# Kernel optimization log

Measured on AMD Instinct MI355X. Metric: run time of the kernel, lower is better.

The kernel has to match this reference:

```python
import math
import jax, jax.numpy as jnp
import numpy as np

B, T, D_MODEL, H, D = 2, 1024, 1024, 16, 64
NUM_LEVELS = int(math.ceil(math.log2(T + 1))) + 1  # 12 for max_seq_len=1024


def _fenwick_level(idx):
    return (idx & -idx).bit_length() - 1


def build_fenwick_masks(T, num_levels):
    """NumPy replica of the torch build_fenwick_masks; returns [L, T, T] float32."""
    j_to_nodes = {}
    for j in range(1, T + 1):
        nodes = []
        idx = j
        while idx <= T:
            nodes.append((idx, _fenwick_level(idx)))
            idx += idx & -idx
        j_to_nodes[j] = nodes
    t_to_query_nodes = {}
    for t in range(1, T + 1):
        s = set()
        idx = t
        while idx > 0:
            s.add(idx)
            idx -= idx & -idx
        t_to_query_nodes[t] = s
    masks = np.zeros((num_levels, T, T), dtype=np.float32)
    for t in range(1, T + 1):
        qn = t_to_query_nodes[t]
        for j in range(1, t + 1):
            for node_idx, node_level in j_to_nodes[j]:
                if node_idx in qn:
                    masks[min(node_level, num_levels - 1), t - 1, j - 1] = 1.0
                    break
    return masks


def setup_inputs() -> dict:
    key = jax.random.key(0)
    ks = jax.random.split(key, 8)
    s = 0.02
    return {
        "x": jax.random.normal(ks[0], (B, T, D_MODEL), jnp.float32),
        "qw": jax.random.normal(ks[1], (D_MODEL, H * D), jnp.float32) * s,
        "qb": jnp.zeros((H * D,), jnp.float32),
        "kw": jax.random.normal(ks[2], (D_MODEL, H * D), jnp.float32) * s,
        "kb": jnp.zeros((H * D,), jnp.float32),
        "vw": jax.random.normal(ks[3], (D_MODEL, H * D), jnp.float32) * s,
        "vb": jnp.zeros((H * D,), jnp.float32),
        "lw": jax.random.normal(ks[4], (D_MODEL, H * NUM_LEVELS), jnp.float32) * s,
        "lb": jnp.zeros((H * NUM_LEVELS,), jnp.float32),
        "ow": jax.random.normal(ks[5], (H * D, D_MODEL), jnp.float32) * s,
        "ob": jnp.zeros((D_MODEL,), jnp.float32),
        "level_masks": jnp.asarray(build_fenwick_masks(T, NUM_LEVELS)),
    }


def reference(x, qw, qb, kw, kb, vw, vb, lw, lb, ow, ob, level_masks):
    b, t, _ = x.shape
    phi = lambda a: jax.nn.elu(a) + 1.0  # ELU+1 feature map
    # projections -> [B, H, T, D]
    Q = (x @ qw + qb).reshape(b, t, H, D).transpose(0, 2, 1, 3)
    K = (x @ kw + kb).reshape(b, t, H, D).transpose(0, 2, 1, 3)
    V = (x @ vw + vb).reshape(b, t, H, D).transpose(0, 2, 1, 3)
    Qp, Kp = phi(Q), phi(K)
    # per-level mixing weights: [B, H, T, L]
    logits = (x @ lw + lb).reshape(b, t, H, NUM_LEVELS).transpose(0, 2, 1, 3)
    w = jax.nn.softmax(logits, axis=-1)
    # scores are level-independent in the original; compute once
    S = jnp.einsum('bhid,bhjd->bhij', Qp, Kp)
    # sum_l w_l * mask_l folded into one weighted mask: [B, H, T, T]
    Mw = jnp.einsum('bhil,lij->bhij', w, level_masks)
    Sm = S * Mw
    num = jnp.einsum('bhij,bhjd->bhid', Sm, V)
    den = jnp.maximum(jnp.sum(Sm, axis=-1, keepdims=True), 1e-6)
    out = (num / den).transpose(0, 2, 1, 3).reshape(b, t, H * D)
    return out @ ow + ob
```

## Files before the change

kernel.cpp:

```cpp
#include <hip/hip_runtime.h>
#include <math.h>

typedef __bf16 bf16;
typedef __attribute__((ext_vector_type(4))) __bf16 bf16x4;
typedef __attribute__((ext_vector_type(8))) __bf16 bf16x8;
typedef __attribute__((ext_vector_type(4))) float f32x4;

#define B_SZ 2
#define T_SZ 1024
#define DM_SZ 1024
#define H_SZ 16
#define D_SZ 64
#define L_SZ 12
#define M_ROWS 2048
#define N_PAD 3328

__device__ __forceinline__ f32x4 mfma_16x16x32(bf16x8 a, bf16x8 b, f32x4 c) {
  return __builtin_amdgcn_mfma_f32_16x16x32_bf16(a, b, c, 0, 0, 0);
}

__device__ __forceinline__ void gload_lds16(const bf16* g, bf16* l) {
  __builtin_amdgcn_global_load_lds((const __attribute__((address_space(1))) void*)g,
                                   (__attribute__((address_space(3))) void*)l,
                                   16, 0, 0);
}

__global__ __launch_bounds__(256) void k_prep(
    const float* __restrict__ x, bf16* __restrict__ xb,
    const float* __restrict__ qw, const float* __restrict__ kw,
    const float* __restrict__ vw, const float* __restrict__ ow,
    const float* __restrict__ lw,
    bf16* __restrict__ wqkvT, bf16* __restrict__ owT) {
  const int z = blockIdx.z;
  const int t = threadIdx.x;
  if (z == 5) {
    const size_t base = ((size_t)blockIdx.y * 16 + blockIdx.x) * 8192 + t * 32;
#pragma unroll
    for (int u = 0; u < 4; ++u) {
      const float* p = x + base + u * 8;
      f32x4 a = *(const f32x4*)p;
      f32x4 b = *(const f32x4*)(p + 4);
      bf16x8 o;
#pragma unroll
      for (int e = 0; e < 4; ++e) { o[e] = (bf16)a[e]; o[e + 4] = (bf16)b[e]; }
      *(bf16x8*)(xb + base + u * 8) = o;
    }
    return;
  }
  __shared__ __align__(16) bf16 tile[64][66];
  const float* in; bf16* out; int C = 1024;
  if (z == 0)      { in = qw; out = wqkvT; }
  else if (z == 1) { in = kw; out = wqkvT + (size_t)1024 * DM_SZ; }
  else if (z == 2) { in = vw; out = wqkvT + (size_t)2048 * DM_SZ; }
  else if (z == 3) { in = ow; out = owT; }
  else             { in = lw; out = wqkvT + (size_t)3072 * DM_SZ; C = 192;
                     if (blockIdx.x >= 3) return; }
  const int tc = blockIdx.x * 64;
  const int tr = blockIdx.y * 64;
  const int r = t >> 2;
  const int c4 = (t & 3) << 4;
  const float* src = in + (size_t)(tr + r) * C + tc + c4;
  f32x4 f0 = *(const f32x4*)(src);
  f32x4 f1 = *(const f32x4*)(src + 4);
  f32x4 f2 = *(const f32x4*)(src + 8);
  f32x4 f3 = *(const f32x4*)(src + 12);
#pragma unroll
  for (int e = 0; e < 4; ++e) {
    tile[r][c4 + e]      = (bf16)f0[e];
    tile[r][c4 + 4 + e]  = (bf16)f1[e];
    tile[r][c4 + 8 + e]  = (bf16)f2[e];
    tile[r][c4 + 12 + e] = (bf16)f3[e];
  }
  __syncthreads();
  bf16x8 w0, w1;
#pragma unroll
  for (int e = 0; e < 8; ++e) { w0[e] = tile[c4 + e][r]; w1[e] = tile[c4 + 8 + e][r]; }
  bf16* dst = out + (size_t)(tc + r) * DM_SZ + tr + c4;
  *(bf16x8*)(dst) = w0;
  *(bf16x8*)(dst + 8) = w1;
}

__global__ __launch_bounds__(256) void k_gemm_qkvl(
    const bf16* __restrict__ A, const bf16* __restrict__ Wt,
    const float* __restrict__ qb, const float* __restrict__ kb,
    const float* __restrict__ vb, const float* __restrict__ lb,
    bf16* __restrict__ Qp, bf16* __restrict__ Kp,
    bf16* __restrict__ VTg, float* __restrict__ logit) {
  __shared__ __align__(16) char smem[65536];
  bf16* Asb = (bf16*)smem;
  bf16* Bsb = Asb + 16384;
  const int nb = blockIdx.x * 128;
  const int mb = blockIdx.y * 128;
  const int t = threadIdx.x;
  const int wv = t >> 6;
  const int lane = t & 63;
  const int l16 = lane & 15;
  const int quad = lane >> 4;
  const int wm = (wv & 1) * 64;
  const int wn = (wv >> 1) * 64;

  const int trow = t >> 3;
  const int tcol = (t & 7) * 8;

  const f32x4 zero4 = {0.f, 0.f, 0.f, 0.f};
  f32x4 acc[4][4];
#pragma unroll
  for (int i = 0; i < 4; ++i)
#pragma unroll
    for (int j = 0; j < 4; ++j) acc[i][j] = zero4;

  const bf16* ag = A + (size_t)(mb + trow) * DM_SZ + tcol;
  const bf16* bg = Wt + (size_t)(nb + trow) * DM_SZ + tcol;

  auto stage = [&](int k0, int buf) {
    bf16* As = Asb + buf * 8192;
    bf16* Bs = Bsb + buf * 8192;
#pragma unroll
    for (int i = 0; i < 4; ++i)
      gload_lds16(ag + (size_t)i * 32 * DM_SZ + k0, As + i * 2048 + t * 8);
#pragma unroll
    for (int i = 0; i < 4; ++i)
      gload_lds16(bg + (size_t)i * 32 * DM_SZ + k0, Bs + i * 2048 + t * 8);
  };

  stage(0, 0);
  for (int k0 = 0; k0 < DM_SZ; k0 += 64) {
    const int cur = (k0 >> 6) & 1;
    __syncthreads();
    if (k0 + 64 < DM_SZ) stage(k0 + 64, cur ^ 1);
    const bf16* As = Asb + cur * 8192;
    const bf16* Bs = Bsb + cur * 8192;
#pragma unroll
    for (int ks = 0; ks < 2; ++ks) {
      bf16x8 af[4];
#pragma unroll
      for (int mi = 0; mi < 4; ++mi)
        af[mi] = *(const bf16x8*)(As + (wm + mi * 16 + l16) * 64 + ks * 32 + quad * 8);
#pragma unroll
      for (int ni = 0; ni < 4; ++ni) {
        bf16x8 bfr = *(const bf16x8*)(Bs + (wn + ni * 16 + l16) * 64 + ks * 32 + quad * 8);
#pragma unroll
        for (int mi = 0; mi < 4; ++mi)
          acc[mi][ni] = mfma_16x16x32(af[mi], bfr, acc[mi][ni]);
      }
    }
  }

  const int seg = nb >> 10;
  if (seg < 2) {
    const float* bias = seg == 0 ? qb : kb;
    bf16* outp = seg == 0 ? Qp : Kp;
    const int c0 = (nb & 1023) + wn;
#pragma unroll
    for (int ni = 0; ni < 4; ++ni) {
      const int col = c0 + ni * 16 + l16;
      const float bv = bias[col];
#pragma unroll
      for (int mi = 0; mi < 4; ++mi) {
#pragma unroll
        for (int r = 0; r < 4; ++r) {
          const int row = mb + wm + mi * 16 + quad * 4 + r;
          float v = acc[mi][ni][r] + bv;
          v = (v > 0.f) ? (v + 1.f) : __expf(v);
          outp[(size_t)row * DM_SZ + col] = (bf16)v;
        }
      }
    }
  } else if (seg == 2) {
    bf16* Trt = (bf16*)smem;
    const int cb = nb - 2048;
    __syncthreads();
#pragma unroll
    for (int ni = 0; ni < 4; ++ni) {
      const int nloc = wn + ni * 16 + l16;
      const float bv = vb[cb + nloc];
#pragma unroll
      for (int mi = 0; mi < 4; ++mi) {
        const int mloc = wm + mi * 16 + quad * 4;
        bf16x4 pk;
#pragma unroll
        for (int r = 0; r < 4; ++r) pk[r] = (bf16)(acc[mi][ni][r] + bv);
        *(bf16x4*)&Trt[nloc * 136 + mloc] = pk;
      }
    }
    __syncthreads();
    const int dn = t >> 1, ch = t & 1;
    const int bq = mb >> 10;
    const int m0g = mb & 1023;
    bf16* dst = VTg + ((size_t)(bq * 1024 + cb + dn)) * T_SZ + m0g + ch * 64;
    const bf16* srcl = Trt + dn * 136 + ch * 64;
#pragma unroll
    for (int e = 0; e < 8; ++e)
      *(bf16x8*)(dst + e * 8) = *(const bf16x8*)(srcl + e * 8);
  } else {
    const int lc0 = (nb - 3072) + wn;
#pragma unroll
    for (int ni = 0; ni < 4; ++ni) {
      const int lcol = lc0 + ni * 16 + l16;
      if (lcol < H_SZ * L_SZ) {
        const float bv = lb[lcol];
#pragma unroll
        for (int mi = 0; mi < 4; ++mi) {
#pragma unroll
          for (int r = 0; r < 4; ++r) {
            const int row = mb + wm + mi * 16 + quad * 4 + r;
            logit[(size_t)row * (H_SZ * L_SZ) + lcol] = acc[mi][ni][r] + bv;
          }
        }
      }
    }
  }
}

__global__ __launch_bounds__(256) void k_build(const bf16* __restrict__ Kp,
                                               const bf16* __restrict__ VTg,
                                               float* __restrict__ Hbuf,
                                               float* __restrict__ ksumbuf) {
  __shared__ __align__(16) bf16 KTs[64][72];
  __shared__ __align__(16) bf16 VTs[64][72];
  const int idx = blockIdx.x;
  const int bh = idx & 31;
  const int jt = idx >> 5;
  const int b = bh >> 4, h = bh & 15;
  const int t = threadIdx.x;
  const int wv = t >> 6, lane = t & 63, l16 = lane & 15, quad = lane >> 4;
  const int r = t >> 2, c = (t & 3) << 4;

  const bf16* vp = VTg + ((size_t)bh * 64 + r) * T_SZ + jt * 64 + c;
  bf16x8 v0 = *(const bf16x8*)vp;
  bf16x8 v1 = *(const bf16x8*)(vp + 8);
  const bf16* kp = Kp + ((size_t)b * T_SZ + jt * 64 + r) * DM_SZ + h * 64 + c;
  bf16x8 k0 = *(const bf16x8*)kp;
  bf16x8 k1 = *(const bf16x8*)(kp + 8);
  *(bf16x8*)&VTs[r][c] = v0;
  *(bf16x8*)&VTs[r][c + 8] = v1;
#pragma unroll
  for (int e = 0; e < 8; ++e) { KTs[c + e][r] = k0[e]; KTs[c + 8 + e][r] = k1[e]; }
  __syncthreads();

  if (t < 64) {
    float s = 0.f;
#pragma unroll
    for (int j = 0; j < 64; ++j) s += (float)KTs[t][j];
    ksumbuf[((size_t)bh * 16 + jt) * 64 + t] = s;
  }

  const f32x4 zero4 = {0.f, 0.f, 0.f, 0.f};
  f32x4 acc[4];
#pragma unroll
  for (int tn = 0; tn < 4; ++tn) acc[tn] = zero4;
#pragma unroll
  for (int ks = 0; ks < 2; ++ks) {
    bf16x8 af = *(const bf16x8*)&VTs[wv * 16 + l16][ks * 32 + quad * 8];
#pragma unroll
    for (int tn = 0; tn < 4; ++tn) {
      bf16x8 bfr = *(const bf16x8*)&KTs[tn * 16 + l16][ks * 32 + quad * 8];
      acc[tn] = mfma_16x16x32(af, bfr, acc[tn]);
    }
  }
  float* hp = Hbuf + ((size_t)bh * 16 + jt) * 4096;
#pragma unroll
  for (int tn = 0; tn < 4; ++tn)
#pragma unroll
    for (int rr = 0; rr < 4; ++rr)
      hp[(wv * 16 + quad * 4 + rr) * 64 + tn * 16 + l16] = acc[tn][rr];
}

__global__ __launch_bounds__(256) void k_attn(const bf16* __restrict__ Qp,
                                              const bf16* __restrict__ Kp,
                                              const bf16* __restrict__ VTg,
                                              const float* __restrict__ Lg,
                                              const float* __restrict__ Hbuf,
                                              const float* __restrict__ ksumbuf,
                                              bf16* __restrict__ O) {
  __shared__ __align__(16) bf16 Ks[64][72];
  __shared__ __align__(16) bf16 VTs[64][72];
  __shared__ __align__(16) bf16 Ms[4][64][72];
  __shared__ __align__(16) bf16 Pl[4][16][80];
  __shared__ __align__(16) bf16 Bdvs[16][72];
  __shared__ float Ws[64 * L_SZ];
  __shared__ float q63s[64];
  __shared__ float y63s[64];
  __shared__ float dsum63s;

  const int idx = blockIdx.x;
  const int s = idx >> 5;
  const int bh = idx & 31;
  const int it = (s < 8) ? (15 - s) : (s - 8);
  const int b = bh >> 4;
  const int h = bh & 15;
  const int i0 = it * 64;
  const int t = threadIdx.x;
  const int wv = t >> 6;
  const int lane = t & 63;
  const int l16 = lane & 15;
  const int quad = lane >> 4;
  const int m0 = wv * 16;
  const size_t base_bt = (size_t)b * T_SZ;

  for (int i = t; i < 16 * 72; i += 256) ((short*)Bdvs)[i] = 0;
  if (t < 64) y63s[t] = 0.f;
  if (t == 0) dsum63s = 0.f;

  const bf16* qptr = Qp + (base_bt + i0 + m0 + l16) * DM_SZ + h * 64 + quad * 8;
  const bf16x8 aq0 = *(const bf16x8*)(qptr);
  const bf16x8 aq1 = *(const bf16x8*)(qptr + 32);

  if (t < 64) q63s[t] = (float)Qp[(base_bt + i0 + 63) * DM_SZ + h * 64 + t];

  const int sr = t >> 2;
  const int sc = (t & 3) << 4;
  const bf16* kpg = Kp + (base_bt + i0 + sr) * DM_SZ + h * 64 + sc;
  const bf16x8 kv0 = *(const bf16x8*)(kpg);
  const bf16x8 kv1 = *(const bf16x8*)(kpg + 8);
  const bf16* vpg = VTg + ((size_t)bh * 64 + sr) * T_SZ + i0 + sc;
  const bf16x8 vv0 = *(const bf16x8*)(vpg);
  const bf16x8 vv1 = *(const bf16x8*)(vpg + 8);

  if (t < 64) {
    const float* lp = Lg + (base_bt + i0 + t) * (H_SZ * L_SZ) + h * L_SZ;
    float v[L_SZ];
    float m = -1e30f;
#pragma unroll
    for (int l = 0; l < L_SZ; ++l) { v[l] = lp[l]; m = fmaxf(m, v[l]); }
    float sum = 0.f;
#pragma unroll
    for (int l = 0; l < L_SZ; ++l) { v[l] = __expf(v[l] - m); sum += v[l]; }
    const float inv = 1.f / sum;
#pragma unroll
    for (int l = 0; l < L_SZ; ++l) Ws[t * L_SZ + l] = v[l] * inv;
  }

  __syncthreads();

  *(bf16x8*)&Ks[sr][sc] = kv0;
  *(bf16x8*)&Ks[sr][sc + 8] = kv1;
  *(bf16x8*)&VTs[sr][sc] = vv0;
  *(bf16x8*)&VTs[sr][sc + 8] = vv1;

  const int il_base = m0 + quad * 4;
  const f32x4 zero4 = {0.f, 0.f, 0.f, 0.f};
  f32x4 accn[4];
#pragma unroll
  for (int tn = 0; tn < 4; ++tn) accn[tn] = zero4;
  float den[4] = {0.f, 0.f, 0.f, 0.f};

  if (it > 0) {
    const float* hb = Hbuf + (size_t)bh * 16 * 4096;
    const float* ksb = ksumbuf + (size_t)bh * 16 * 64;
    f32x4 m63a[4];
#pragma unroll
    for (int i = 0; i < 4; ++i) m63a[i] = zero4;
    float dv63 = 0.f;
    int x = it;
    while (x > 0) {
      const int g = __builtin_ctz((unsigned)x);
      const int lo = x - (1 << g);
      f32x4 ma[4];
#pragma unroll
      for (int i = 0; i < 4; ++i) ma[i] = zero4;
      float dva = 0.f;
      for (int jt = lo; jt < x; ++jt) {
        const float wB = Ws[63 * L_SZ + 6 + (31 - __clz((unsigned)((it + 1) ^ jt)))];
        const float* lp = hb + jt * 4096 + t * 16;
#pragma unroll
        for (int i = 0; i < 4; ++i) {
          f32x4 hv = *(const f32x4*)(lp + i * 4);
#pragma unroll
          for (int e = 0; e < 4; ++e) {
            ma[i][e] += hv[e];
            m63a[i][e] += wB * hv[e];
          }
        }
        if (t < 64) {
          const float ksv = ksb[jt * 64 + t];
          dva += ksv;
          dv63 += wB * ksv;
        }
      }
      bf16x8 o0, o1;
#pragma unroll
      for (int e = 0; e < 4; ++e) {
        o0[e] = (bf16)ma[0][e]; o0[e + 4] = (bf16)ma[1][e];
        o1[e] = (bf16)ma[2][e]; o1[e + 4] = (bf16)ma[3][e];
      }
      *(bf16x8*)&Ms[g][t >> 2][(t & 3) << 4] = o0;
      *(bf16x8*)&Ms[g][t >> 2][((t & 3) << 4) + 8] = o1;
      if (t < 64) Bdvs[g][t] = (bf16)dva;
      x = lo;
    }
    float p63 = 0.f;
    const int d1b = (t & 3) << 4;
#pragma unroll
    for (int i = 0; i < 4; ++i)
#pragma unroll
      for (int e = 0; e < 4; ++e) p63 += q63s[d1b + i * 4 + e] * m63a[i][e];
    p63 += __shfl_xor(p63, 1, 64);
    p63 += __shfl_xor(p63, 2, 64);
    if ((t & 3) == 0) y63s[t >> 2] = p63;
    if (t < 64) {
      float pd = q63s[t] * dv63;
      pd += __shfl_xor(pd, 1, 64);
      pd += __shfl_xor(pd, 2, 64);
      pd += __shfl_xor(pd, 4, 64);
      pd += __shfl_xor(pd, 8, 64);
      pd += __shfl_xor(pd, 16, 64);
      pd += __shfl_xor(pd, 32, 64);
      if (t == 0) dsum63s = pd;
    }
  }
  __syncthreads();

  if (it > 0) {
    int x = it;
    while (x > 0) {
      const int g = __builtin_ctz((unsigned)x);
      f32x4 ya[4];
#pragma unroll
      for (int tn = 0; tn < 4; ++tn) ya[tn] = zero4;
#pragma unroll
      for (int ks = 0; ks < 2; ++ks) {
        const bf16x8 af = ks ? aq1 : aq0;
#pragma unroll
        for (int tn = 0; tn < 4; ++tn) {
          bf16x8 bfr = *(const bf16x8*)&Ms[g][tn * 16 + l16][ks * 32 + quad * 8];
          ya[tn] = mfma_16x16x32(af, bfr, ya[tn]);
        }
      }
      float wg[4];
#pragma unroll
      for (int r = 0; r < 4; ++r) {
        const int il = il_base + r;
        wg[r] = (il == 63) ? 0.f : Ws[il * L_SZ + 6 + g];
      }
#pragma unroll
      for (int tn = 0; tn < 4; ++tn)
#pragma unroll
        for (int r = 0; r < 4; ++r) accn[tn][r] += wg[r] * ya[tn][r];
      x -= 1 << g;
    }
    f32x4 da = zero4;
#pragma unroll
    for (int ks = 0; ks < 2; ++ks) {
      const bf16x8 af = ks ? aq1 : aq0;
      bf16x8 bfr = *(const bf16x8*)&Bdvs[l16][ks * 32 + quad * 8];
      da = mfma_16x16x32(af, bfr, da);
    }
#pragma unroll
    for (int r = 0; r < 4; ++r) {
      const int il = il_base + r;
      const float wd = (il == 63) ? 0.f : Ws[il * L_SZ + 6 + (l16 & 3)];
      den[r] += wd * da[r];
    }
  }

  {
    f32x4 sacc[4];
    __builtin_amdgcn_s_setprio(1);
#pragma unroll
    for (int tn = 0; tn < 4; ++tn) {
      sacc[tn] = zero4;
      bf16x8 bk0 = *(const bf16x8*)&Ks[tn * 16 + l16][quad * 8];
      bf16x8 bk1 = *(const bf16x8*)&Ks[tn * 16 + l16][32 + quad * 8];
      sacc[tn] = mfma_16x16x32(aq0, bk0, sacc[tn]);
      sacc[tn] = mfma_16x16x32(aq1, bk1, sacc[tn]);
    }
    __builtin_amdgcn_s_setprio(0);
#pragma unroll
    for (int tn = 0; tn < 4; ++tn) {
#pragma unroll
      for (int r = 0; r < 4; ++r) {
        const int il = il_base + r;
        const int ig = i0 + il;
        const int jg = i0 + tn * 16 + l16;
        float p = 0.f;
        if (jg <= ig) {
          const int lvl = 31 - __clz((unsigned)((ig + 1) ^ jg));
          p = sacc[tn][r] * Ws[il * L_SZ + lvl];
        }
        den[r] += p;
        Pl[wv][quad * 4 + r][(tn * 16 + l16) ^ (quad << 4)] = (bf16)p;
      }
    }
    __builtin_amdgcn_s_setprio(1);
#pragma unroll
    for (int ks = 0; ks < 2; ++ks) {
      bf16x8 apf = *(const bf16x8*)&Pl[wv][l16][(ks * 32 + quad * 8) ^ ((l16 >> 2) << 4)];
#pragma unroll
      for (int tn = 0; tn < 4; ++tn) {
        bf16x8 bvf = *(const bf16x8*)&VTs[tn * 16 + l16][ks * 32 + quad * 8];
        accn[tn] = mfma_16x16x32(apf, bvf, accn[tn]);
      }
    }
    __builtin_amdgcn_s_setprio(0);
  }

#pragma unroll
  for (int r = 0; r < 4; ++r) {
    float d = den[r];
    d += __shfl_xor(d, 1, 64);
    d += __shfl_xor(d, 2, 64);
    d += __shfl_xor(d, 4, 64);
    d += __shfl_xor(d, 8, 64);
    den[r] = d;
  }
  if (il_base + 3 == 63) den[3] += dsum63s;
#pragma unroll
  for (int r = 0; r < 4; ++r) den[r] = fmaxf(den[r], 1e-6f);

#pragma unroll
  for (int tn = 0; tn < 4; ++tn) {
#pragma unroll
    for (int r = 0; r < 4; ++r) {
      const int il = il_base + r;
      float v = accn[tn][r];
      if (il == 63) v += y63s[tn * 16 + l16];
      O[(base_bt + i0 + il) * DM_SZ + h * 64 + tn * 16 + l16] =
          (bf16)(v / den[r]);
    }
  }
}

__global__ __launch_bounds__(256) void k_gemm_out(const bf16* __restrict__ A,
                                                  const bf16* __restrict__ Wt,
                                                  const float* __restrict__ ob,
                                                  float* __restrict__ out) {
  __shared__ __align__(16) bf16 As[2][64 * 64];
  __shared__ __align__(16) bf16 Bs[2][64 * 64];
  const int nb = blockIdx.x * 64;
  const int mb = blockIdx.y * 64;
  const int t = threadIdx.x;
  const int wv = t >> 6;
  const int lane = t & 63;
  const int l16 = lane & 15;
  const int quad = lane >> 4;
  const int wm = wv * 16;

  const int trow = t >> 3;
  const int tcol = (t & 7) * 8;

  const f32x4 zero4 = {0.f, 0.f, 0.f, 0.f};
  f32x4 acc[4];
#pragma unroll
  for (int j = 0; j < 4; ++j) acc[j] = zero4;

  const bf16* ag = A + (size_t)(mb + trow) * DM_SZ + tcol;
  const bf16* bg = Wt + (size_t)(nb + trow) * DM_SZ + tcol;

  auto stageg = [&](int k0, int buf) {
    gload_lds16(ag + k0, As[buf] + t * 8);
    gload_lds16(ag + (size_t)32 * DM_SZ + k0, As[buf] + 2048 + t * 8);
    gload_lds16(bg + k0, Bs[buf] + t * 8);
    gload_lds16(bg + (size_t)32 * DM_SZ + k0, Bs[buf] + 2048 + t * 8);
  };

  stageg(0, 0);
  for (int k0 = 0; k0 < DM_SZ; k0 += 64) {
    const int cur = (k0 >> 6) & 1;
    __syncthreads();
    if (k0 + 64 < DM_SZ) stageg(k0 + 64, cur ^ 1);
#pragma unroll
    for (int ks = 0; ks < 2; ++ks) {
      bf16x8 af = *(const bf16x8*)(As[cur] + (wm + l16) * 64 + ks * 32 + quad * 8);
#pragma unroll
      for (int ni = 0; ni < 4; ++ni) {
        bf16x8 bfr = *(const bf16x8*)(Bs[cur] + (ni * 16 + l16) * 64 + ks * 32 + quad * 8);
        acc[ni] = mfma_16x16x32(af, bfr, acc[ni]);
      }
    }
  }
#pragma unroll
  for (int ni = 0; ni < 4; ++ni) {
    const int col = nb + ni * 16 + l16;
    const float bv = ob[col];
#pragma unroll
    for (int r = 0; r < 4; ++r) {
      const int row = mb + wm + quad * 4 + r;
      out[(size_t)row * DM_SZ + col] = acc[ni][r] + bv;
    }
  }
}

extern "C" void kernel_launch(void* const* d_in, const int* in_sizes, int n_in,
                              void* d_out, int out_size, void* d_ws, size_t ws_size,
                              hipStream_t stream) {
  (void)in_sizes; (void)n_in; (void)out_size; (void)ws_size;
  const float* x  = (const float*)d_in[0];
  const float* qw = (const float*)d_in[1];
  const float* qb = (const float*)d_in[2];
  const float* kw = (const float*)d_in[3];
  const float* kb = (const float*)d_in[4];
  const float* vw = (const float*)d_in[5];
  const float* vb = (const float*)d_in[6];
  const float* lw = (const float*)d_in[7];
  const float* lb = (const float*)d_in[8];
  const float* ow = (const float*)d_in[9];
  const float* ob = (const float*)d_in[10];

  char* ws = (char*)d_ws;
  size_t off = 0;
  auto alloc = [&](size_t bytes) -> char* {
    char* p = ws + off;
    off += (bytes + 255) & ~(size_t)255;
    return p;
  };
  bf16* xb     = (bf16*)alloc((size_t)M_ROWS * DM_SZ * 2);
  bf16* wqkvT  = (bf16*)alloc((size_t)N_PAD * DM_SZ * 2);
  bf16* owT    = (bf16*)alloc((size_t)DM_SZ * DM_SZ * 2);
  bf16* Qp     = (bf16*)alloc((size_t)M_ROWS * DM_SZ * 2);
  bf16* Kpb    = (bf16*)alloc((size_t)M_ROWS * DM_SZ * 2);
  bf16* VTg    = (bf16*)alloc((size_t)M_ROWS * DM_SZ * 2);
  bf16* attn   = (bf16*)alloc((size_t)M_ROWS * DM_SZ * 2);
  float* logit = (float*)alloc((size_t)M_ROWS * H_SZ * L_SZ * 4);
  float* Hbuf  = (float*)alloc((size_t)32 * 16 * 4096 * 4);
  float* ksumb = (float*)alloc((size_t)32 * 16 * 64 * 4);

  const dim3 blk(256);
  k_prep<<<dim3(16, 16, 6), blk, 0, stream>>>(x, xb, qw, kw, vw, ow, lw, wqkvT, owT);
  k_gemm_qkvl<<<dim3(N_PAD / 128, M_ROWS / 128), blk, 0, stream>>>(
      xb, wqkvT, qb, kb, vb, lb, Qp, Kpb, VTg, logit);
  k_build<<<dim3(32 * 16), blk, 0, stream>>>(Kpb, VTg, Hbuf, ksumb);
  k_attn<<<dim3((T_SZ / 64) * B_SZ * H_SZ), blk, 0, stream>>>(
      Qp, Kpb, VTg, logit, Hbuf, ksumb, attn);
  k_gemm_out<<<dim3(DM_SZ / 64, M_ROWS / 64), blk, 0, stream>>>(attn, owT, ob, (float*)d_out);
}
```

Baseline: 179.4 us.

## Use triple-buffered BK=32 pipeline with explicit vmcnt waits in projection GEMMs

Both the QKV/logit projection GEMM and the output GEMM switch from a double-buffered K-step of 64 to a triple-buffered K-step of 32. Each iteration waits with a partial s_waitcnt vmcnt so the prefetch for the step two ahead stays in flight, then uses a raw s_barrier instead of __syncthreads. The aim is to hide global-to-LDS load latency better and to cut LDS usage (64KB to 48KB in the first GEMM) so more blocks can be resident. The cost is twice as many barriers per K and hand-written waitcnt logic that has to match the number of outstanding loads exactly.

```diff
diff --git a/kernel.cpp b/kernel.cpp
--- a/kernel.cpp
+++ b/kernel.cpp
@@ -86,9 +86,9 @@
     const float* __restrict__ vb, const float* __restrict__ lb,
     bf16* __restrict__ Qp, bf16* __restrict__ Kp,
     bf16* __restrict__ VTg, float* __restrict__ logit) {
-  __shared__ __align__(16) char smem[65536];
+  __shared__ __align__(16) char smem[49152];
   bf16* Asb = (bf16*)smem;
-  bf16* Bsb = Asb + 16384;
+  bf16* Bsb = Asb + 12288;
   const int nb = blockIdx.x * 128;
   const int mb = blockIdx.y * 128;
   const int t = threadIdx.x;
@@ -99,8 +99,8 @@
   const int wm = (wv & 1) * 64;
   const int wn = (wv >> 1) * 64;
 
-  const int trow = t >> 3;
-  const int tcol = (t & 7) * 8;
+  const int trow = t >> 2;
+  const int tcol = (t & 3) * 8;
 
   const f32x4 zero4 = {0.f, 0.f, 0.f, 0.f};
   f32x4 acc[4][4];
@@ -113,38 +113,46 @@
   const bf16* bg = Wt + (size_t)(nb + trow) * DM_SZ + tcol;
 
   auto stage = [&](int k0, int buf) {
-    bf16* As = Asb + buf * 8192;
-    bf16* Bs = Bsb + buf * 8192;
-#pragma unroll
-    for (int i = 0; i < 4; ++i)
-      gload_lds16(ag + (size_t)i * 32 * DM_SZ + k0, As + i * 2048 + t * 8);
-#pragma unroll
-    for (int i = 0; i < 4; ++i)
-      gload_lds16(bg + (size_t)i * 32 * DM_SZ + k0, Bs + i * 2048 + t * 8);
+    bf16* As = Asb + buf * 4096;
+    bf16* Bs = Bsb + buf * 4096;
+    gload_lds16(ag + k0, As + t * 8);
+    gload_lds16(ag + (size_t)64 * DM_SZ + k0, As + 2048 + t * 8);
+    gload_lds16(bg + k0, Bs + t * 8);
+    gload_lds16(bg + (size_t)64 * DM_SZ + k0, Bs + 2048 + t * 8);
   };
 
+  auto computeStep = [&](int buf) {
+    const bf16* As = Asb + buf * 4096;
+    const bf16* Bs = Bsb + buf * 4096;
+    bf16x8 af[4];
+#pragma unroll
+    for (int mi = 0; mi < 4; ++mi)
+      af[mi] = *(const bf16x8*)(As + (wm + mi * 16 + l16) * 32 + quad * 8);
+#pragma unroll
+    for (int ni = 0; ni < 4; ++ni) {
+      bf16x8 bfr = *(const bf16x8*)(Bs + (wn + ni * 16 + l16) * 32 + quad * 8);
+#pragma unroll
+      for (int mi = 0; mi < 4; ++mi)
+        acc[mi][ni] = mfma_16x16x32(af[mi], bfr, acc[mi][ni]);
+    }
+  };
+
   stage(0, 0);
-  for (int k0 = 0; k0 < DM_SZ; k0 += 64) {
-    const int cur = (k0 >> 6) & 1;
-    __syncthreads();
-    if (k0 + 64 < DM_SZ) stage(k0 + 64, cur ^ 1);
-    const bf16* As = Asb + cur * 8192;
-    const bf16* Bs = Bsb + cur * 8192;
-#pragma unroll
-    for (int ks = 0; ks < 2; ++ks) {
-      bf16x8 af[4];
-#pragma unroll
-      for (int mi = 0; mi < 4; ++mi)
-        af[mi] = *(const bf16x8*)(As + (wm + mi * 16 + l16) * 64 + ks * 32 + quad * 8);
-#pragma unroll
-      for (int ni = 0; ni < 4; ++ni) {
-        bf16x8 bfr = *(const bf16x8*)(Bs + (wn + ni * 16 + l16) * 64 + ks * 32 + quad * 8);
-#pragma unroll
-        for (int mi = 0; mi < 4; ++mi)
-          acc[mi][ni] = mfma_16x16x32(af[mi], bfr, acc[mi][ni]);
-      }
-    }
-  }
+  stage(32, 1);
+  int cb = 0, sb = 2;
+  for (int k0 = 0; k0 < DM_SZ - 32; k0 += 32) {
+    asm volatile("s_waitcnt vmcnt(4)" ::: "memory");
+    __builtin_amdgcn_s_barrier();
+    __builtin_amdgcn_sched_barrier(0);
+    if (k0 + 64 < DM_SZ) stage(k0 + 64, sb);
+    computeStep(cb);
+    cb = (cb == 2) ? 0 : cb + 1;
+    sb = (sb == 2) ? 0 : sb + 1;
+  }
+  asm volatile("s_waitcnt vmcnt(0)" ::: "memory");
+  __builtin_amdgcn_s_barrier();
+  __builtin_amdgcn_sched_barrier(0);
+  computeStep(cb);
 
   const int seg = nb >> 10;
   if (seg < 2) {
@@ -168,12 +176,12 @@
     }
   } else if (seg == 2) {
     bf16* Trt = (bf16*)smem;
-    const int cb = nb - 2048;
+    const int cb2 = nb - 2048;
     __syncthreads();
 #pragma unroll
     for (int ni = 0; ni < 4; ++ni) {
       const int nloc = wn + ni * 16 + l16;
-      const float bv = vb[cb + nloc];
+      const float bv = vb[cb2 + nloc];
 #pragma unroll
       for (int mi = 0; mi < 4; ++mi) {
         const int mloc = wm + mi * 16 + quad * 4;
@@ -187,7 +195,7 @@
     const int dn = t >> 1, ch = t & 1;
     const int bq = mb >> 10;
     const int m0g = mb & 1023;
-    bf16* dst = VTg + ((size_t)(bq * 1024 + cb + dn)) * T_SZ + m0g + ch * 64;
+    bf16* dst = VTg + ((size_t)(bq * 1024 + cb2 + dn)) * T_SZ + m0g + ch * 64;
     const bf16* srcl = Trt + dn * 136 + ch * 64;
 #pragma unroll
     for (int e = 0; e < 8; ++e)
@@ -525,8 +533,8 @@
                                                   const bf16* __restrict__ Wt,
                                                   const float* __restrict__ ob,
                                                   float* __restrict__ out) {
-  __shared__ __align__(16) bf16 As[2][64 * 64];
-  __shared__ __align__(16) bf16 Bs[2][64 * 64];
+  __shared__ __align__(16) bf16 As[3][2048];
+  __shared__ __align__(16) bf16 Bs[3][2048];
   const int nb = blockIdx.x * 64;
   const int mb = blockIdx.y * 64;
   const int t = threadIdx.x;
@@ -536,8 +544,8 @@
   const int quad = lane >> 4;
   const int wm = wv * 16;
 
-  const int trow = t >> 3;
-  const int tcol = (t & 7) * 8;
+  const int trow = t >> 2;
+  const int tcol = (t & 3) * 8;
 
   const f32x4 zero4 = {0.f, 0.f, 0.f, 0.f};
   f32x4 acc[4];
@@ -549,26 +557,34 @@
 
   auto stageg = [&](int k0, int buf) {
     gload_lds16(ag + k0, As[buf] + t * 8);
-    gload_lds16(ag + (size_t)32 * DM_SZ + k0, As[buf] + 2048 + t * 8);
     gload_lds16(bg + k0, Bs[buf] + t * 8);
-    gload_lds16(bg + (size_t)32 * DM_SZ + k0, Bs[buf] + 2048 + t * 8);
   };
+  auto computeStep = [&](int buf) {
+    bf16x8 af = *(const bf16x8*)(As[buf] + (wm + l16) * 32 + quad * 8);
+#pragma unroll
+    for (int ni = 0; ni < 4; ++ni) {
+      bf16x8 bfr = *(const bf16x8*)(Bs[buf] + (ni * 16 + l16) * 32 + quad * 8);
+      acc[ni] = mfma_16x16x32(af, bfr, acc[ni]);
+    }
+  };
 
   stageg(0, 0);
-  for (int k0 = 0; k0 < DM_SZ; k0 += 64) {
-    const int cur = (k0 >> 6) & 1;
-    __syncthreads();
-    if (k0 + 64 < DM_SZ) stageg(k0 + 64, cur ^ 1);
-#pragma unroll
-    for (int ks = 0; ks < 2; ++ks) {
-      bf16x8 af = *(const bf16x8*)(As[cur] + (wm + l16) * 64 + ks * 32 + quad * 8);
-#pragma unroll
-      for (int ni = 0; ni < 4; ++ni) {
-        bf16x8 bfr = *(const bf16x8*)(Bs[cur] + (ni * 16 + l16) * 64 + ks * 32 + quad * 8);
-        acc[ni] = mfma_16x16x32(af, bfr, acc[ni]);
-      }
-    }
-  }
+  stageg(32, 1);
+  int cb = 0, sb = 2;
+  for (int k0 = 0; k0 < DM_SZ - 32; k0 += 32) {
+    asm volatile("s_waitcnt vmcnt(2)" ::: "memory");
+    __builtin_amdgcn_s_barrier();
+    __builtin_amdgcn_sched_barrier(0);
+    if (k0 + 64 < DM_SZ) stageg(k0 + 64, sb);
+    computeStep(cb);
+    cb = (cb == 2) ? 0 : cb + 1;
+    sb = (sb == 2) ? 0 : sb + 1;
+  }
+  asm volatile("s_waitcnt vmcnt(0)" ::: "memory");
+  __builtin_amdgcn_s_barrier();
+  __builtin_amdgcn_sched_barrier(0);
+  computeStep(cb);
+
 #pragma unroll
   for (int ni = 0; ni < 4; ++ni) {
     const int col = nb + ni * 16 + l16;
```

Measured after the change: 171.9 us, median of 2. -4.2%, faster.

## Load GEMM MFMA fragments directly from global memory, bypassing LDS staging

Applied to the files above, without the earlier changes.

Both the QKV/level projection GEMM and the output projection GEMM stop staging tiles through double-buffered LDS with global_load_lds and barriers. Each lane now loads its MFMA fragments straight from global memory into registers, using a two-stage register double buffer across k-steps. This removes LDS traffic and per-iteration __syncthreads. In exchange, operands shared across waves are fetched redundantly through the caches, and every row access is a strided 16-byte load rather than a coalesced tile load.

```diff
diff --git a/kernel.cpp b/kernel.cpp
--- a/kernel.cpp
+++ b/kernel.cpp
@@ -86,9 +86,7 @@
     const float* __restrict__ vb, const float* __restrict__ lb,
     bf16* __restrict__ Qp, bf16* __restrict__ Kp,
     bf16* __restrict__ VTg, float* __restrict__ logit) {
-  __shared__ __align__(16) char smem[65536];
-  bf16* Asb = (bf16*)smem;
-  bf16* Bsb = Asb + 16384;
+  __shared__ __align__(16) bf16 Trt[128 * 136];
   const int nb = blockIdx.x * 128;
   const int mb = blockIdx.y * 128;
   const int t = threadIdx.x;
@@ -99,9 +97,6 @@
   const int wm = (wv & 1) * 64;
   const int wn = (wv >> 1) * 64;
 
-  const int trow = t >> 3;
-  const int tcol = (t & 7) * 8;
-
   const f32x4 zero4 = {0.f, 0.f, 0.f, 0.f};
   f32x4 acc[4][4];
 #pragma unroll
@@ -109,42 +104,43 @@
 #pragma unroll
     for (int j = 0; j < 4; ++j) acc[i][j] = zero4;
 
-  const bf16* ag = A + (size_t)(mb + trow) * DM_SZ + tcol;
-  const bf16* bg = Wt + (size_t)(nb + trow) * DM_SZ + tcol;
-
-  auto stage = [&](int k0, int buf) {
-    bf16* As = Asb + buf * 8192;
-    bf16* Bs = Bsb + buf * 8192;
-#pragma unroll
-    for (int i = 0; i < 4; ++i)
-      gload_lds16(ag + (size_t)i * 32 * DM_SZ + k0, As + i * 2048 + t * 8);
-#pragma unroll
-    for (int i = 0; i < 4; ++i)
-      gload_lds16(bg + (size_t)i * 32 * DM_SZ + k0, Bs + i * 2048 + t * 8);
-  };
-
-  stage(0, 0);
-  for (int k0 = 0; k0 < DM_SZ; k0 += 64) {
-    const int cur = (k0 >> 6) & 1;
-    __syncthreads();
-    if (k0 + 64 < DM_SZ) stage(k0 + 64, cur ^ 1);
-    const bf16* As = Asb + cur * 8192;
-    const bf16* Bs = Bsb + cur * 8192;
-#pragma unroll
-    for (int ks = 0; ks < 2; ++ks) {
-      bf16x8 af[4];
-#pragma unroll
-      for (int mi = 0; mi < 4; ++mi)
-        af[mi] = *(const bf16x8*)(As + (wm + mi * 16 + l16) * 64 + ks * 32 + quad * 8);
-#pragma unroll
-      for (int ni = 0; ni < 4; ++ni) {
-        bf16x8 bfr = *(const bf16x8*)(Bs + (wn + ni * 16 + l16) * 64 + ks * 32 + quad * 8);
-#pragma unroll
-        for (int mi = 0; mi < 4; ++mi)
-          acc[mi][ni] = mfma_16x16x32(af[mi], bfr, acc[mi][ni]);
-      }
-    }
-  }
+  const bf16* ap[4];
+  const bf16* bp[4];
+#pragma unroll
+  for (int mi = 0; mi < 4; ++mi)
+    ap[mi] = A + (size_t)(mb + wm + mi * 16 + l16) * DM_SZ + quad * 8;
+#pragma unroll
+  for (int ni = 0; ni < 4; ++ni)
+    bp[ni] = Wt + (size_t)(nb + wn + ni * 16 + l16) * DM_SZ + quad * 8;
+
+  bf16x8 a0[4], b0[4], a1[4], b1[4];
+
+#define LOADF(AA, BB, K0)                                       \
+  {                                                             \
+    _Pragma("unroll") for (int i = 0; i < 4; ++i)               \
+        AA[i] = *(const bf16x8*)(ap[i] + (K0));                 \
+    _Pragma("unroll") for (int i = 0; i < 4; ++i)               \
+        BB[i] = *(const bf16x8*)(bp[i] + (K0));                 \
+  }
+#define STEP(AA, BB)                                            \
+  {                                                             \
+    _Pragma("unroll") for (int ni = 0; ni < 4; ++ni)            \
+        _Pragma("unroll") for (int mi = 0; mi < 4; ++mi)        \
+            acc[mi][ni] = mfma_16x16x32(AA[mi], BB[ni], acc[mi][ni]); \
+  }
+
+  LOADF(a0, b0, 0);
+  for (int k0 = 0; k0 < DM_SZ - 64; k0 += 64) {
+    LOADF(a1, b1, k0 + 32);
+    STEP(a0, b0);
+    LOADF(a0, b0, k0 + 64);
+    STEP(a1, b1);
+  }
+  LOADF(a1, b1, DM_SZ - 32);
+  STEP(a0, b0);
+  STEP(a1, b1);
+#undef LOADF
+#undef STEP
 
   const int seg = nb >> 10;
   if (seg < 2) {
@@ -167,13 +163,11 @@
       }
     }
   } else if (seg == 2) {
-    bf16* Trt = (bf16*)smem;
-    const int cb = nb - 2048;
-    __syncthreads();
+    const int cb2 = nb - 2048;
 #pragma unroll
     for (int ni = 0; ni < 4; ++ni) {
       const int nloc = wn + ni * 16 + l16;
-      const float bv = vb[cb + nloc];
+      const float bv = vb[cb2 + nloc];
 #pragma unroll
       for (int mi = 0; mi < 4; ++mi) {
         const int mloc = wm + mi * 16 + quad * 4;
@@ -187,7 +181,7 @@
     const int dn = t >> 1, ch = t & 1;
     const int bq = mb >> 10;
     const int m0g = mb & 1023;
-    bf16* dst = VTg + ((size_t)(bq * 1024 + cb + dn)) * T_SZ + m0g + ch * 64;
+    bf16* dst = VTg + ((size_t)(bq * 1024 + cb2 + dn)) * T_SZ + m0g + ch * 64;
     const bf16* srcl = Trt + dn * 136 + ch * 64;
 #pragma unroll
     for (int e = 0; e < 8; ++e)
@@ -525,8 +519,6 @@
                                                   const bf16* __restrict__ Wt,
                                                   const float* __restrict__ ob,
                                                   float* __restrict__ out) {
-  __shared__ __align__(16) bf16 As[2][64 * 64];
-  __shared__ __align__(16) bf16 Bs[2][64 * 64];
   const int nb = blockIdx.x * 64;
   const int mb = blockIdx.y * 64;
   const int t = threadIdx.x;
@@ -536,39 +528,44 @@
   const int quad = lane >> 4;
   const int wm = wv * 16;
 
-  const int trow = t >> 3;
-  const int tcol = (t & 7) * 8;
-
   const f32x4 zero4 = {0.f, 0.f, 0.f, 0.f};
   f32x4 acc[4];
 #pragma unroll
   for (int j = 0; j < 4; ++j) acc[j] = zero4;
 
-  const bf16* ag = A + (size_t)(mb + trow) * DM_SZ + tcol;
-  const bf16* bg = Wt + (size_t)(nb + trow) * DM_SZ + tcol;
-
-  auto stageg = [&](int k0, int buf) {
-    gload_lds16(ag + k0, As[buf] + t * 8);
-    gload_lds16(ag + (size_t)32 * DM_SZ + k0, As[buf] + 2048 + t * 8);
-    gload_lds16(bg + k0, Bs[buf] + t * 8);
-    gload_lds16(bg + (size_t)32 * DM_SZ + k0, Bs[buf] + 2048 + t * 8);
-  };
-
-  stageg(0, 0);
-  for (int k0 = 0; k0 < DM_SZ; k0 += 64) {
-    const int cur = (k0 >> 6) & 1;
-    __syncthreads();
-    if (k0 + 64 < DM_SZ) stageg(k0 + 64, cur ^ 1);
-#pragma unroll
-    for (int ks = 0; ks < 2; ++ks) {
-      bf16x8 af = *(const bf16x8*)(As[cur] + (wm + l16) * 64 + ks * 32 + quad * 8);
-#pragma unroll
-      for (int ni = 0; ni < 4; ++ni) {
-        bf16x8 bfr = *(const bf16x8*)(Bs[cur] + (ni * 16 + l16) * 64 + ks * 32 + quad * 8);
-        acc[ni] = mfma_16x16x32(af, bfr, acc[ni]);
-      }
-    }
-  }
+  const bf16* apo = A + (size_t)(mb + wm + l16) * DM_SZ + quad * 8;
+  const bf16* bpo[4];
+#pragma unroll
+  for (int ni = 0; ni < 4; ++ni)
+    bpo[ni] = Wt + (size_t)(nb + ni * 16 + l16) * DM_SZ + quad * 8;
+
+  bf16x8 a0, a1, b0[4], b1[4];
+
+#define LOADFO(AS, BS, K0)                                      \
+  {                                                             \
+    AS = *(const bf16x8*)(apo + (K0));                          \
+    _Pragma("unroll") for (int i = 0; i < 4; ++i)               \
+        BS[i] = *(const bf16x8*)(bpo[i] + (K0));                \
+  }
+#define STEPO(AS, BS)                                           \
+  {                                                             \
+    _Pragma("unroll") for (int ni = 0; ni < 4; ++ni)            \
+        acc[ni] = mfma_16x16x32(AS, BS[ni], acc[ni]);           \
+  }
+
+  LOADFO(a0, b0, 0);
+  for (int k0 = 0; k0 < DM_SZ - 64; k0 += 64) {
+    LOADFO(a1, b1, k0 + 32);
+    STEPO(a0, b0);
+    LOADFO(a0, b0, k0 + 64);
+    STEPO(a1, b1);
+  }
+  LOADFO(a1, b1, DM_SZ - 32);
+  STEPO(a0, b0);
+  STEPO(a1, b1);
+#undef LOADFO
+#undef STEPO
+
 #pragma unroll
   for (int ni = 0; ni < 4; ++ni) {
     const int col = nb + ni * 16 + l16;
```

Measured after the change: 233.6 us. 30.2% more time.
